# Kernel optimization log

Measured on AMD Instinct MI355X. Metric: run time of the kernel, lower is better.

Reference implementation:

```python
import jax, jax.numpy as jnp
import numpy as np

N, E, B = 100000, 1600000, 1024
F, H, C = 9, 4, 32
CH, L = 30, 20

def _leaky(x, slope):
    return jnp.where(x >= 0, x, slope * x)

def _add_self_loops(edge_index, n):
    ar = jnp.arange(n, dtype=edge_index.dtype)
    return jnp.concatenate([edge_index, jnp.stack([ar, ar])], axis=1)

def _gat_conv(x, edge_index, W, att_src, att_dst, bias):
    # PyG GATConv, concat heads, eval mode (no attn dropout), self loops
    n = x.shape[0]
    ei = _add_self_loops(edge_index, n)
    src, dst = ei[0], ei[1]
    h = (x @ W).reshape(n, H, C)                      # [N,H,C]
    a_s = jnp.sum(h * att_src, axis=-1)               # [N,H]
    a_d = jnp.sum(h * att_dst, axis=-1)               # [N,H]
    e = _leaky(a_s[src] + a_d[dst], 0.2)              # [Etot,H]
    m = jax.ops.segment_max(e, dst, num_segments=n)
    ex = jnp.exp(e - m[dst])
    s = jax.ops.segment_sum(ex, dst, num_segments=n)
    alpha = ex / (s[dst] + 1e-16)                     # softmax per dst node/head
    msg = h[src] * alpha[:, :, None]                  # [Etot,H,C]
    out = jax.ops.segment_sum(msg, dst, num_segments=n)
    return out.reshape(n, H * C) + bias

def _gcn_conv(x, edge_index, W, bias):
    # PyG GCNConv: self loops + symmetric normalization
    n = x.shape[0]
    ei = _add_self_loops(edge_index, n)
    src, dst = ei[0], ei[1]
    deg = jax.ops.segment_sum(jnp.ones(ei.shape[1], x.dtype), dst, num_segments=n)
    dinv = jnp.where(deg > 0, jax.lax.rsqrt(deg), 0.0)
    norm = dinv[src] * dinv[dst]                      # [Etot]
    h = x @ W
    out = jax.ops.segment_sum(h[src] * norm[:, None], dst, num_segments=n)
    return out + bias

def _global_mean_pool(x, batch, b):
    s = jax.ops.segment_sum(x, batch, num_segments=b)
    cnt = jax.ops.segment_sum(jnp.ones(x.shape[0], x.dtype), batch, num_segments=b)
    return s / jnp.maximum(cnt, 1.0)[:, None]

def _conv1d(x, w, b):
    # x: [B,Cin,L], w: [Cout,Cin,K], VALID conv
    y = jax.lax.conv_general_dilated(x, w, (1,), 'VALID',
                                     dimension_numbers=('NCH', 'OIH', 'NCH'))
    return y + b[None, :, None]

def _bn_eval(x, g, be, m, v):
    return (x - m[None, :, None]) * jax.lax.rsqrt(v[None, :, None] + 1e-5) * g[None, :, None] + be[None, :, None]

def _forward(x, seq_data, W_gat, att_src, att_dst, b_gat, W2, b2, W3, b3,
             conv1_w, conv1_b, conv2_w, conv2_b,
             bn1_g, bn1_b, bn1_m, bn1_v, bn2_g, bn2_b, bn2_m, bn2_v,
             fc1_W, fc1_b, fus_W, fus_b, cls1_W, cls1_b, cls3_W, cls3_b,
             edge_index, batch):
    slope = 0.01  # nn.LeakyReLU default
    # graph branch
    g = _leaky(_gat_conv(x, edge_index, W_gat, att_src, att_dst, b_gat), slope)
    g = _leaky(_gcn_conv(g, edge_index, W2, b2), slope)
    g = _leaky(_gcn_conv(g, edge_index, W3, b3), slope)
    g = _global_mean_pool(g, batch, B)                # [B,128]
    # sequence branch (eval mode: dropout = identity, BN uses running stats)
    s = _conv1d(seq_data, conv1_w, conv1_b)           # [B,64,18]
    s = _leaky(_bn_eval(s, bn1_g, bn1_b, bn1_m, bn1_v), slope)
    s = _conv1d(s, conv2_w, conv2_b)                  # [B,64,16]
    s = _leaky(_bn_eval(s, bn2_g, bn2_b, bn2_m, bn2_v), slope)
    s = s.reshape(s.shape[0], -1) @ fc1_W + fc1_b     # [B,64]
    # fusion + classifier
    comb = jnp.concatenate([g, s], axis=1)            # [B,192]
    comb = _leaky(comb @ fus_W + fus_b, slope)
    comb = _leaky(comb @ cls1_W + cls1_b, slope)
    return comb @ cls3_W + cls3_b                     # [B,1]

def setup_inputs():
    key = jax.random.key(0)
    ks = jax.random.split(key, 20)
    rn = lambda k, s, sc=0.1: jax.random.normal(k, s, dtype=jnp.float32) * sc
    return {
        'x': rn(ks[0], (N, F), 1.0),
        'edge_index': jax.random.randint(ks[1], (2, E), 0, N, dtype=jnp.int32),
        'batch': jnp.sort(jax.random.randint(ks[2], (N,), 0, B, dtype=jnp.int32)),
        'seq_data': rn(ks[3], (B, CH, L), 1.0),
        'W_gat': rn(ks[4], (F, H * C)), 'att_src': rn(ks[5], (H, C)),
        'att_dst': rn(ks[6], (H, C)), 'b_gat': jnp.zeros(H * C, jnp.float32),
        'W2': rn(ks[7], (H * C, 64)), 'b2': jnp.zeros(64, jnp.float32),
        'W3': rn(ks[8], (64, 128)), 'b3': jnp.zeros(128, jnp.float32),
        'conv1_w': rn(ks[9], (64, CH, 3)), 'conv1_b': jnp.zeros(64, jnp.float32),
        'conv2_w': rn(ks[10], (64, 64, 3)), 'conv2_b': jnp.zeros(64, jnp.float32),
        'bn1_g': jnp.ones(64, jnp.float32), 'bn1_b': jnp.zeros(64, jnp.float32),
        'bn1_m': jnp.zeros(64, jnp.float32), 'bn1_v': jnp.ones(64, jnp.float32),
        'bn2_g': jnp.ones(64, jnp.float32), 'bn2_b': jnp.zeros(64, jnp.float32),
        'bn2_m': jnp.zeros(64, jnp.float32), 'bn2_v': jnp.ones(64, jnp.float32),
        'fc1_W': rn(ks[11], (16 * 64, 64)), 'fc1_b': jnp.zeros(64, jnp.float32),
        'fus_W': rn(ks[12], (192, 128)), 'fus_b': jnp.zeros(128, jnp.float32),
        'cls1_W': rn(ks[13], (128, 64)), 'cls1_b': jnp.zeros(64, jnp.float32),
        'cls3_W': rn(ks[14], (64, 1)), 'cls3_b': jnp.zeros(1, jnp.float32),
    }

def reference(x, edge_index, batch, seq_data, W_gat, att_src, att_dst, b_gat,
              W2, b2, W3, b3, conv1_w, conv1_b, conv2_w, conv2_b,
              bn1_g, bn1_b, bn1_m, bn1_v, bn2_g, bn2_b, bn2_m, bn2_v,
              fc1_W, fc1_b, fus_W, fus_b, cls1_W, cls1_b, cls3_W, cls3_b):
    return _forward(x, seq_data, W_gat, att_src, att_dst, b_gat, W2, b2, W3, b3,
                    conv1_w, conv1_b, conv2_w, conv2_b,
                    bn1_g, bn1_b, bn1_m, bn1_v, bn2_g, bn2_b, bn2_m, bn2_v,
                    fc1_W, fc1_b, fus_W, fus_b, cls1_W, cls1_b, cls3_W, cls3_b,
                    edge_index, batch)
```

## Files before the change

### kernel.cpp

```cpp
#include <hip/hip_runtime.h>

#define NND 100000
#define NED 1600000
#define NB  1024
#define FEAT 9
#define HC 128
#define NBUCK ((NND + 511) / 512)
#define BCAP 12288u
#define BINCHUNK 4096
#define BIN_NBLK ((NED + BINCHUNK - 1) / BINCHUNK)

typedef unsigned short u16;

__device__ __forceinline__ void atomAdd(float* p, float v) {
    __hip_atomic_fetch_add(p, v, __ATOMIC_RELAXED, __HIP_MEMORY_SCOPE_AGENT);
}
__device__ __forceinline__ unsigned atomAddU(unsigned* p, unsigned v) {
    return __hip_atomic_fetch_add(p, v, __ATOMIC_RELAXED, __HIP_MEMORY_SCOPE_AGENT);
}
__device__ __forceinline__ float leaky(float v, float s) { return v >= 0.f ? v : s * v; }
__device__ __forceinline__ float bf2f(u16 u) {
    union { unsigned i; float f; } x; x.i = ((unsigned)u) << 16; return x.f;
}
__device__ __forceinline__ u16 f2bf(float f) {
    union { float f; unsigned i; } x; x.f = f;
    return (u16)((x.i + 0x7fffu + ((x.i >> 16) & 1u)) >> 16);
}
__device__ __forceinline__ float bflo(unsigned u) {
    union { unsigned i; float f; } x; x.i = u << 16; return x.f;
}
__device__ __forceinline__ float bfhi(unsigned u) {
    union { unsigned i; float f; } x; x.i = u & 0xffff0000u; return x.f;
}

__global__ void k_matt(const float* __restrict__ Wg, const float* __restrict__ attS,
                       const float* __restrict__ attD, float* __restrict__ M) {
    int t = threadIdx.x;
    if (t >= 72) return;
    int d = t >= 36 ? 1 : 0;
    int q = t - 36 * d;
    int f = q >> 2, h = q & 3;
    const float* av = d ? attD : attS;
    float s = 0.f;
#pragma unroll
    for (int c = 0; c < 32; ++c) s += Wg[f * HC + h * 32 + c] * av[h * 32 + c];
    M[d * 36 + q] = s;
}

__global__ void k_w2t(const float* __restrict__ W2, const float* __restrict__ W3,
                      u16* __restrict__ w2t, u16* __restrict__ w3t,
                      unsigned* __restrict__ bktCur) {
    int i = blockIdx.x * 256 + threadIdx.x;
    int n = i >> 7, k = i & 127;
    w2t[i] = f2bf(W2[k * 64 + n]);
    int n3 = i >> 6, k3 = i & 63;
    w3t[i] = f2bf(W3[k3 * 128 + n3]);
    if (i < NBUCK) bktCur[i] = (unsigned)i * BCAP;
}

__global__ void k_att(const float* __restrict__ x, const float* __restrict__ M,
                      u16* __restrict__ rec, float* __restrict__ a_d) {
    __shared__ float Ms[36], Md[36];
    int t = threadIdx.x;
    if (t < 36) Ms[t] = M[t];
    else if (t < 72) Md[t - 36] = M[t];
    __syncthreads();
    int n = blockIdx.x * 256 + t;
    if (n >= NND) return;
    float xv[FEAT];
#pragma unroll
    for (int f = 0; f < FEAT; ++f) xv[f] = x[n * FEAT + f];
    float s0 = 0, s1 = 0, s2 = 0, s3 = 0, d0 = 0, d1 = 0, d2 = 0, d3 = 0;
#pragma unroll
    for (int f = 0; f < FEAT; ++f) {
        float xf = xv[f];
        s0 += xf * Ms[f * 4 + 0]; s1 += xf * Ms[f * 4 + 1];
        s2 += xf * Ms[f * 4 + 2]; s3 += xf * Ms[f * 4 + 3];
        d0 += xf * Md[f * 4 + 0]; d1 += xf * Md[f * 4 + 1];
        d2 += xf * Md[f * 4 + 2]; d3 += xf * Md[f * 4 + 3];
    }
    u16 v[16];
#pragma unroll
    for (int f = 0; f < FEAT; ++f) v[f] = f2bf(xv[f]);
    v[9] = 0; v[10] = 0; v[11] = 0;
    v[12] = f2bf(s0); v[13] = f2bf(s1); v[14] = f2bf(s2); v[15] = f2bf(s3);
    unsigned pk[8];
#pragma unroll
    for (int i = 0; i < 8; ++i) pk[i] = (unsigned)v[2 * i] | ((unsigned)v[2 * i + 1] << 16);
    uint4* rp = (uint4*)(rec + (size_t)n * 16);
    rp[0] = make_uint4(pk[0], pk[1], pk[2], pk[3]);
    rp[1] = make_uint4(pk[4], pk[5], pk[6], pk[7]);
    ((float4*)a_d)[n] = make_float4(d0, d1, d2, d3);
}

__global__ __launch_bounds__(256) void k_bin(const int* __restrict__ ei,
                                             unsigned* __restrict__ bktCursor,
                                             unsigned* __restrict__ staging) {
    __shared__ unsigned hist[NBUCK];
    __shared__ unsigned gbase[NBUCK];
    int t = threadIdx.x;
    if (t < NBUCK) hist[t] = 0;
    __syncthreads();
    int base = blockIdx.x * BINCHUNK;
    int lim = NED - base;
    int srcv[16], dstv[16];
#pragma unroll
    for (int k = 0; k < 16; ++k) {
        int i = t + k * 256;
        if (i < lim) {
            srcv[k] = ei[base + i];
            dstv[k] = ei[NED + base + i];
            atomicAdd(&hist[dstv[k] >> 9], 1u);
        } else dstv[k] = -1;
    }
    __syncthreads();
    if (t < NBUCK) {
        unsigned c = hist[t];
        gbase[t] = c ? atomAddU(&bktCursor[t], c) : 0u;
    }
    __syncthreads();
    if (t < NBUCK) hist[t] = 0;
    __syncthreads();
#pragma unroll
    for (int k = 0; k < 16; ++k) {
        if (dstv[k] >= 0) {
            int bk = dstv[k] >> 9;
            unsigned off = atomicAdd(&hist[bk], 1u);
            staging[gbase[bk] + off] = ((unsigned)(dstv[k] & 511) << 17) | (unsigned)srcv[k];
        }
    }
}

__global__ __launch_bounds__(512) void k_place(const unsigned* __restrict__ bktCur,
                                               const unsigned* __restrict__ staging,
                                               unsigned* __restrict__ csr,
                                               unsigned* __restrict__ rowptr,
                                               u16* __restrict__ degA,
                                               float* __restrict__ dinv) {
    __shared__ unsigned lh[512];
    __shared__ unsigned ls[512];
    int b = blockIdx.x, t = threadIdx.x;
    unsigned lo = (unsigned)b * BCAP;
    unsigned n = bktCur[b] - lo;
    lh[t] = 0;
    __syncthreads();
    for (unsigned i = t; i < n; i += 512) atomicAdd(&lh[staging[lo + i] >> 17], 1u);
    __syncthreads();
    unsigned v = lh[t];
    ls[t] = v;
    __syncthreads();
    for (int off = 1; off < 512; off <<= 1) {
        unsigned u = (t >= off) ? ls[t - off] : 0u;
        __syncthreads();
        ls[t] += u;
        __syncthreads();
    }
    unsigned excl = ls[t] - v;
    int node = b * 512 + t;
    if (node < NND) {
        rowptr[node] = lo + excl;
        degA[node] = (u16)v;
        dinv[node] = rsqrtf((float)v + 1.f);
    }
    __syncthreads();
    lh[t] = excl;
    __syncthreads();
    for (unsigned i = t; i < n; i += 512) {
        unsigned p = staging[lo + i];
        unsigned pos = atomicAdd(&lh[p >> 17], 1u);
        csr[lo + pos] = p & 0x1FFFFu;
    }
}

__global__ __launch_bounds__(256) void k_gat_g(const unsigned* __restrict__ rowptr,
                                               const u16* __restrict__ degA,
                                               const unsigned* __restrict__ csr,
                                               const u16* __restrict__ rec,
                                               const float* __restrict__ a_d,
                                               float* __restrict__ z) {
    int n = blockIdx.x * 4 + (threadIdx.x >> 6);
    int l = threadIdx.x & 63;
    int e = l >> 2;
    int h = l & 3;
    unsigned e0 = rowptr[n];
    int m = (int)degA[n] + 1;
    float adh = a_d[n * 4 + h];
    float acc0 = 0, acc1 = 0, acc2 = 0, acc3 = 0, acc4 = 0, acc5 = 0, acc6 = 0, acc7 = 0, acc8 = 0;
    float den = 0.f;
    const uint4* recp = (const uint4*)rec;
    for (int c = 0; c < m; c += 16) {
        int idx = c + e;
        bool act = idx < m;
        int src = n;
        if (act && idx > 0) src = (int)csr[e0 + idx - 1];
        uint4 lo = recp[(size_t)src * 2];
        uint4 hi = recp[(size_t)src * 2 + 1];
        unsigned pair = (h & 2) ? hi.w : hi.z;
        float asf = (h & 1) ? bfhi(pair) : bflo(pair);
        float w = __expf(leaky(asf + adh, 0.2f));
        if (!act) w = 0.f;
        den += w;
        acc0 += w * bflo(lo.x); acc1 += w * bfhi(lo.x);
        acc2 += w * bflo(lo.y); acc3 += w * bfhi(lo.y);
        acc4 += w * bflo(lo.z); acc5 += w * bfhi(lo.z);
        acc6 += w * bflo(lo.w); acc7 += w * bfhi(lo.w);
        acc8 += w * bflo(hi.x);
    }
#pragma unroll
    for (int mask = 4; mask <= 32; mask <<= 1) {
        den  += __shfl_xor(den,  mask, 64);
        acc0 += __shfl_xor(acc0, mask, 64);
        acc1 += __shfl_xor(acc1, mask, 64);
        acc2 += __shfl_xor(acc2, mask, 64);
        acc3 += __shfl_xor(acc3, mask, 64);
        acc4 += __shfl_xor(acc4, mask, 64);
        acc5 += __shfl_xor(acc5, mask, 64);
        acc6 += __shfl_xor(acc6, mask, 64);
        acc7 += __shfl_xor(acc7, mask, 64);
        acc8 += __shfl_xor(acc8, mask, 64);
    }
    if (l < 4) {
        float inv = 1.f / (den + 1e-16f);
        float* zp = z + (size_t)n * 36 + h * 9;
        zp[0] = acc0 * inv; zp[1] = acc1 * inv; zp[2] = acc2 * inv;
        zp[3] = acc3 * inv; zp[4] = acc4 * inv; zp[5] = acc5 * inv;
        zp[6] = acc6 * inv; zp[7] = acc7 * inv; zp[8] = acc8 * inv;
    }
}

typedef __attribute__((ext_vector_type(8))) short bfrag;
typedef __attribute__((ext_vector_type(4))) float ffrag;
__global__ __launch_bounds__(256) void k_fused_h2(const float* __restrict__ z,
                                                  const float* __restrict__ Wg,
                                                  const float* __restrict__ bg,
                                                  const u16* __restrict__ w2t,
                                                  const float* __restrict__ dinv,
                                                  u16* __restrict__ h2) {
    __shared__ float zL[64 * 36];
    __shared__ float Wf[FEAT * HC];
    __shared__ float bgs[HC];
    __shared__ u16 g1L[64 * 136];
    int t = threadIdx.x;
    int n0 = blockIdx.x * 64;
    for (int i = t; i < 64 * 36; i += 256) {
        int row = i / 36;
        zL[i] = (n0 + row < NND) ? z[(size_t)(n0 + row) * 36 + (i - row * 36)] : 0.f;
    }
    for (int i = t; i < FEAT * HC; i += 256) Wf[i] = Wg[i];
    if (t < HC) bgs[t] = bg[t];
    __syncthreads();
    for (int e = t; e < 64 * 128; e += 256) {
        int row = e >> 7, col = e & 127;
        int h = col >> 5;
        float acc = bgs[col];
        const float* zr = zL + row * 36 + h * 9;
#pragma unroll
        for (int f = 0; f < 9; ++f) acc += zr[f] * Wf[f * 128 + col];
        g1L[row * 136 + col] = f2bf(leaky(acc, 0.01f));
    }
    __syncthreads();
    int l = t & 63, wv = t >> 6;
    int mr = l & 15, quad = l >> 4;
    union U { uint4 u; bfrag v; };
    bfrag a[4];
#pragma unroll
    for (int ks = 0; ks < 4; ++ks) {
        U uu; uu.u = *(const uint4*)(g1L + (wv * 16 + mr) * 136 + ks * 32 + quad * 8);
        a[ks] = uu.v;
    }
    ffrag acc[4];
#pragma unroll
    for (int ct = 0; ct < 4; ++ct) acc[ct] = (ffrag){0.f, 0.f, 0.f, 0.f};
#pragma unroll
    for (int ct = 0; ct < 4; ++ct) {
#pragma unroll
        for (int ks = 0; ks < 4; ++ks) {
            U ub; ub.u = *(const uint4*)(w2t + (ct * 16 + mr) * 128 + ks * 32 + quad * 8);
            acc[ct] = __builtin_amdgcn_mfma_f32_16x16x32_bf16(a[ks], ub.v, acc[ct], 0, 0, 0);
        }
    }
    int rbase = n0 + wv * 16 + quad * 4;
    if (rbase < NND) {
        float4 d4 = *(const float4*)(dinv + rbase);
        const float dv[4] = {d4.x, d4.y, d4.z, d4.w};
#pragma unroll
        for (int ct = 0; ct < 4; ++ct)
#pragma unroll
            for (int r = 0; r < 4; ++r)
                h2[(size_t)(rbase + r) * 64 + ct * 16 + mr] = f2bf(dv[r] * acc[ct][r]);
    }
}

template <int OUTMODE>
__global__ void k_gcn_g(const unsigned* __restrict__ rowptr, const u16* __restrict__ degA,
                        const unsigned* __restrict__ csr,
                        const float* __restrict__ dinv, const u16* __restrict__ hin,
                        const float* __restrict__ bias, u16* __restrict__ hout) {
    int n = blockIdx.x * 4 + (threadIdx.x >> 6);
    int l = threadIdx.x & 63;
    int grp = l >> 4;
    int c = l & 15;
    unsigned e0 = rowptr[n];
    unsigned e1 = e0 + degA[n];
    const uint2* hinU = (const uint2*)hin;
    float a0 = 0, a1 = 0, a2 = 0, a3 = 0;
    if (grp == 0) {
        uint2 u = hinU[(size_t)n * 16 + c];
        a0 = bflo(u.x); a1 = bfhi(u.x); a2 = bflo(u.y); a3 = bfhi(u.y);
    }
    unsigned e = e0;
    for (; e + 8 <= e1; e += 8) {
        unsigned s0 = csr[e + grp];
        unsigned s1 = csr[e + 4 + grp];
        uint2 u0 = hinU[(size_t)s0 * 16 + c];
        uint2 u1 = hinU[(size_t)s1 * 16 + c];
        a0 += bflo(u0.x) + bflo(u1.x); a1 += bfhi(u0.x) + bfhi(u1.x);
        a2 += bflo(u0.y) + bflo(u1.y); a3 += bfhi(u0.y) + bfhi(u1.y);
    }
    for (; e + 4 <= e1; e += 4) {
        unsigned s = csr[e + grp];
        uint2 u = hinU[(size_t)s * 16 + c];
        a0 += bflo(u.x); a1 += bfhi(u.x); a2 += bflo(u.y); a3 += bfhi(u.y);
    }
    if (grp < (int)(e1 - e)) {
        unsigned s = csr[e + grp];
        uint2 u = hinU[(size_t)s * 16 + c];
        a0 += bflo(u.x); a1 += bfhi(u.x); a2 += bflo(u.y); a3 += bfhi(u.y);
    }
#pragma unroll
    for (int mask = 16; mask <= 32; mask <<= 1) {
        a0 += __shfl_xor(a0, mask, 64);
        a1 += __shfl_xor(a1, mask, 64);
        a2 += __shfl_xor(a2, mask, 64);
        a3 += __shfl_xor(a3, mask, 64);
    }
    if (grp == 0) {
        float dn = dinv[n];
        float o0 = dn * a0, o1 = dn * a1, o2 = dn * a2, o3 = dn * a3;
        if (OUTMODE == 1) {
            o0 = leaky(o0 + bias[4 * c],     0.01f) * dn;
            o1 = leaky(o1 + bias[4 * c + 1], 0.01f) * dn;
            o2 = leaky(o2 + bias[4 * c + 2], 0.01f) * dn;
            o3 = leaky(o3 + bias[4 * c + 3], 0.01f) * dn;
        }
        uint2 pk;
        pk.x = (unsigned)f2bf(o0) | ((unsigned)f2bf(o1) << 16);
        pk.y = (unsigned)f2bf(o2) | ((unsigned)f2bf(o3) << 16);
        ((uint2*)hout)[(size_t)n * 16 + c] = pk;
    }
}

__global__ __launch_bounds__(256) void k_gcn2_pool(const u16* __restrict__ agg3,
                                                   const u16* __restrict__ w3t,
                                                   const float* __restrict__ b3,
                                                   const int* __restrict__ batch,
                                                   float* __restrict__ pooled,
                                                   float* __restrict__ cnt) {
    __shared__ u16 rows[64 * 72];
    __shared__ int bts[64];
    __shared__ float b3s[128];
    int t = threadIdx.x;
    int n0 = blockIdx.x * 64;
    int nn = NND - n0; if (nn > 64) nn = 64;
    const uint4* src = (const uint4*)(agg3 + (size_t)n0 * 64);
    for (int i = t; i < 512; i += 256) {
        int r = i >> 3, c8 = i & 7;
        uint4 v = (r < nn) ? src[i] : make_uint4(0u, 0u, 0u, 0u);
        *(uint4*)(rows + r * 72 + c8 * 8) = v;
    }
    if (t < 64) bts[t] = (t < nn) ? batch[n0 + t] : -1;
    if (t < 128) b3s[t] = b3[t];
    __syncthreads();
    int l = t & 63, wv = t >> 6;
    int mr = l & 15, quad = l >> 4;
    union U { uint4 u; bfrag v; };
    bfrag a[2];
#pragma unroll
    for (int ks = 0; ks < 2; ++ks) {
        U uu; uu.u = *(const uint4*)(rows + (wv * 16 + mr) * 72 + ks * 32 + quad * 8);
        a[ks] = uu.v;
    }
    ffrag acc[8];
#pragma unroll
    for (int ct = 0; ct < 8; ++ct) acc[ct] = (ffrag){0.f, 0.f, 0.f, 0.f};
#pragma unroll
    for (int ct = 0; ct < 8; ++ct) {
#pragma unroll
        for (int ks = 0; ks < 2; ++ks) {
            U ub; ub.u = *(const uint4*)(w3t + (ct * 16 + mr) * 64 + ks * 32 + quad * 8);
            acc[ct] = __builtin_amdgcn_mfma_f32_16x16x32_bf16(a[ks], ub.v, acc[ct], 0, 0, 0);
        }
    }
    int rl = wv * 16 + quad * 4;
    int ub = bts[wv * 16];
    bool uni = (ub == bts[wv * 16 + 15]);
#pragma unroll
    for (int ct = 0; ct < 8; ++ct) {
        int col = ct * 16 + mr;
        float bc = b3s[col];
        float g0 = leaky(acc[ct][0] + bc, 0.01f);
        float g1 = leaky(acc[ct][1] + bc, 0.01f);
        float g2 = leaky(acc[ct][2] + bc, 0.01f);
        float g3 = leaky(acc[ct][3] + bc, 0.01f);
        if (uni) {
            float s = g0 + g1 + g2 + g3;
            s += __shfl_xor(s, 16, 64);
            s += __shfl_xor(s, 32, 64);
            if (quad == 0 && ub >= 0) atomAdd(&pooled[ub * 128 + col], s);
        } else {
            float gr[4] = {g0, g1, g2, g3};
            int curb = bts[rl];
            float s = 0.f;
#pragma unroll
            for (int r = 0; r < 4; ++r) {
                int b = bts[rl + r];
                if (b != curb) {
                    if (curb >= 0) atomAdd(&pooled[curb * 128 + col], s);
                    s = 0.f; curb = b;
                }
                s += gr[r];
            }
            if (curb >= 0) atomAdd(&pooled[curb * 128 + col], s);
        }
    }
    if (t < nn) {
        int b = bts[t];
        if (t == 0 || bts[t - 1] != b) {
            int len = 1;
            for (int j = t + 1; j < nn && bts[j] == b; ++j) ++len;
            atomAdd(&cnt[b], (float)len);
        }
    }
}

__global__ void k_seq(const float* __restrict__ seq, const float* __restrict__ w1, const float* __restrict__ c1b,
                      const float* __restrict__ w2, const float* __restrict__ c2b,
                      const float* __restrict__ g1n, const float* __restrict__ b1n,
                      const float* __restrict__ m1n, const float* __restrict__ v1n,
                      const float* __restrict__ g2n, const float* __restrict__ b2n,
                      const float* __restrict__ m2n, const float* __restrict__ v2n,
                      const float* __restrict__ fcW, const float* __restrict__ fcb,
                      float* __restrict__ sfc) {
    __shared__ float xs[30 * 20];
    __shared__ float y1[64 * 18];
    __shared__ float y2[64 * 16];
    __shared__ float red[4][64];
    int t = threadIdx.x;
    int b = blockIdx.x;
    for (int idx = t; idx < 600; idx += 256) xs[idx] = seq[b * 600 + idx];
    __syncthreads();
    for (int idx = t; idx < 64 * 18; idx += 256) {
        int o = idx / 18, l = idx - o * 18;
        float acc = c1b[o];
        for (int i = 0; i < 30; ++i)
#pragma unroll
            for (int k = 0; k < 3; ++k)
                acc += xs[i * 20 + l + k] * w1[o * 90 + i * 3 + k];
        float bn = (acc - m1n[o]) * rsqrtf(v1n[o] + 1e-5f) * g1n[o] + b1n[o];
        y1[idx] = leaky(bn, 0.01f);
    }
    __syncthreads();
    for (int idx = t; idx < 64 * 16; idx += 256) {
        int o = idx >> 4, l = idx & 15;
        float acc = c2b[o];
        for (int i = 0; i < 64; ++i)
#pragma unroll
            for (int k = 0; k < 3; ++k)
                acc += y1[i * 18 + l + k] * w2[o * 192 + i * 3 + k];
        float bn = (acc - m2n[o]) * rsqrtf(v2n[o] + 1e-5f) * g2n[o] + b2n[o];
        y2[idx] = leaky(bn, 0.01f);
    }
    __syncthreads();
    {
        int o = t & 63, part = t >> 6;
        float acc = 0.f;
        for (int j = part * 256; j < part * 256 + 256; ++j)
            acc += y2[j] * fcW[j * 64 + o];
        red[part][o] = acc;
    }
    __syncthreads();
    if (t < 64) sfc[b * 64 + t] = red[0][t] + red[1][t] + red[2][t] + red[3][t] + fcb[t];
}

__global__ void k_final(const float* __restrict__ pooled, const float* __restrict__ cnt,
                        const float* __restrict__ sfc,
                        const float* __restrict__ fusW, const float* __restrict__ fusb,
                        const float* __restrict__ c1W, const float* __restrict__ c1b,
                        const float* __restrict__ c3W, const float* __restrict__ c3b,
                        float* __restrict__ out) {
    __shared__ float comb[192];
    __shared__ float t1[128];
    int t = threadIdx.x;
    int b = blockIdx.x;
    float invc = 1.f / fmaxf(cnt[b], 1.f);
    comb[t] = pooled[b * 128 + t] * invc;
    if (t < 64) comb[128 + t] = sfc[b * 64 + t];
    __syncthreads();
    float acc = fusb[t];
    for (int k = 0; k < 192; ++k) acc += comb[k] * fusW[k * 128 + t];
    t1[t] = leaky(acc, 0.01f);
    __syncthreads();
    if (t < 64) {
        float a2 = c1b[t];
        for (int k = 0; k < 128; ++k) a2 += t1[k] * c1W[k * 64 + t];
        a2 = leaky(a2, 0.01f);
        float p = a2 * c3W[t];
#pragma unroll
        for (int off = 32; off; off >>= 1) p += __shfl_xor(p, off, 64);
        if (t == 0) out[b] = p + c3b[0];
    }
}

extern "C" void kernel_launch(void* const* d_in, const int* in_sizes, int n_in,
                              void* d_out, int out_size, void* d_ws, size_t ws_size,
                              hipStream_t stream) {
    const float* x     = (const float*)d_in[0];
    const int*   ei    = (const int*)d_in[1];
    const int*   batch = (const int*)d_in[2];
    const float* seq   = (const float*)d_in[3];
    const float* Wg    = (const float*)d_in[4];
    const float* attS  = (const float*)d_in[5];
    const float* attD  = (const float*)d_in[6];
    const float* bg    = (const float*)d_in[7];
    const float* W2    = (const float*)d_in[8];
    const float* b2    = (const float*)d_in[9];
    const float* W3    = (const float*)d_in[10];
    const float* b3    = (const float*)d_in[11];
    const float* c1w   = (const float*)d_in[12];
    const float* c1bb  = (const float*)d_in[13];
    const float* c2w   = (const float*)d_in[14];
    const float* c2bb  = (const float*)d_in[15];
    const float* bn1g  = (const float*)d_in[16];
    const float* bn1b  = (const float*)d_in[17];
    const float* bn1m  = (const float*)d_in[18];
    const float* bn1v  = (const float*)d_in[19];
    const float* bn2g  = (const float*)d_in[20];
    const float* bn2b  = (const float*)d_in[21];
    const float* bn2m  = (const float*)d_in[22];
    const float* bn2v  = (const float*)d_in[23];
    const float* fcW   = (const float*)d_in[24];
    const float* fcb   = (const float*)d_in[25];
    const float* fusW  = (const float*)d_in[26];
    const float* fusb  = (const float*)d_in[27];
    const float* cls1W = (const float*)d_in[28];
    const float* cls1b = (const float*)d_in[29];
    const float* cls3W = (const float*)d_in[30];
    const float* cls3b = (const float*)d_in[31];

    char* wsb = (char*)d_ws;
    const size_t N = NND;
    float*    M      = (float*)wsb;
    float*    a_d    = M + 80;
    u16*      rec    = (u16*)(a_d + N * 4);
    float*    dinv   = (float*)(rec + N * 16);
    float*    pooled = dinv + N;
    float*    cnt    = pooled + (size_t)NB * 128;
    unsigned* bktCur = (unsigned*)(cnt + NB);
    unsigned* rowptr = bktCur + 256;
    u16*      degA   = (u16*)(rowptr + N);
    u16*      w2t    = degA + N + 8;
    u16*      w3t    = w2t + 8192;
    unsigned* staging= (unsigned*)(w3t + 8192);
    unsigned* csr    = staging + (size_t)NBUCK * BCAP;
    float*    z      = (float*)(csr + (size_t)NBUCK * BCAP);
    u16*      h2b    = (u16*)(z + N * 36 + 64);
    u16*      g2b    = h2b + N * 64;
    u16*      agg3b  = g2b + N * 64;
    float*    sfc    = (float*)(agg3b + N * 64);

    size_t zero_bytes = ((size_t)NB * 128 + NB) * 4;
    hipMemsetAsync(pooled, 0, zero_bytes, stream);

    k_matt<<<1, 128, 0, stream>>>(Wg, attS, attD, M);
    k_w2t<<<32, 256, 0, stream>>>(W2, W3, w2t, w3t, bktCur);
    k_att<<<(NND + 255) / 256, 256, 0, stream>>>(x, M, rec, a_d);
    k_bin<<<BIN_NBLK, 256, 0, stream>>>(ei, bktCur, staging);
    k_place<<<NBUCK, 512, 0, stream>>>(bktCur, staging, csr, rowptr, degA, dinv);
    k_gat_g<<<NND / 4, 256, 0, stream>>>(rowptr, degA, csr, rec, a_d, z);
    k_fused_h2<<<(NND + 63) / 64, 256, 0, stream>>>(z, Wg, bg, w2t, dinv, h2b);
    k_gcn_g<1><<<NND / 4, 256, 0, stream>>>(rowptr, degA, csr, dinv, h2b, b2, g2b);
    k_gcn_g<0><<<NND / 4, 256, 0, stream>>>(rowptr, degA, csr, dinv, g2b, b2, agg3b);
    k_gcn2_pool<<<(NND + 63) / 64, 256, 0, stream>>>(agg3b, w3t, b3, batch, pooled, cnt);
    k_seq<<<NB, 256, 0, stream>>>(seq, c1w, c1bb, c2w, c2bb, bn1g, bn1b, bn1m, bn1v,
                                  bn2g, bn2b, bn2m, bn2v, fcW, fcb, sfc);
    k_final<<<NB, 128, 0, stream>>>(pooled, cnt, sfc, fusW, fusb, cls1W, cls1b,
                                    cls3W, cls3b, (float*)d_out);
}
```

Measured before the change: 435.3 us.

## Fuse GAT gather into H2 GEMM and second GCN gather into pooling kernel

Merges the GAT attention gather with the following dense transform. Each 64-node block computes its aggregated features into shared memory as bf16 and then runs the Wg projection with MFMA, using a new padded bf16 Wg, instead of scalar FMAs. Likewise, the second GCN neighbor aggregation now runs inside the W3+pool kernel, which removes the z and agg3 intermediate buffers and two launches. The cost is less parallelism per block, since each wave processes 16 nodes serially. The GAT output is also rounded to bf16 before the projection, which adds precision loss.

```diff
diff --git a/kernel.cpp b/kernel.cpp
--- a/kernel.cpp
+++ b/kernel.cpp
@@ -33,6 +33,9 @@
     union { unsigned i; float f; } x; x.i = u & 0xffff0000u; return x.f;
 }
 
+typedef __attribute__((ext_vector_type(8))) short bfrag;
+typedef __attribute__((ext_vector_type(4))) float ffrag;
+
 __global__ void k_matt(const float* __restrict__ Wg, const float* __restrict__ attS,
                        const float* __restrict__ attD, float* __restrict__ M) {
     int t = threadIdx.x;
@@ -48,13 +51,17 @@
 }
 
 __global__ void k_w2t(const float* __restrict__ W2, const float* __restrict__ W3,
+                      const float* __restrict__ Wg,
                       u16* __restrict__ w2t, u16* __restrict__ w3t,
-                      unsigned* __restrict__ bktCur) {
+                      u16* __restrict__ wgt, unsigned* __restrict__ bktCur) {
     int i = blockIdx.x * 256 + threadIdx.x;
     int n = i >> 7, k = i & 127;
     w2t[i] = f2bf(W2[k * 64 + n]);
     int n3 = i >> 6, k3 = i & 63;
     w3t[i] = f2bf(W3[k3 * 128 + n3]);
+    int col = i >> 6, kk = i & 63;
+    int f = kk - 9 * (col >> 5);
+    wgt[i] = (f >= 0 && f < 9) ? f2bf(Wg[f * 128 + col]) : (u16)0;
     if (i < NBUCK) bktCur[i] = (unsigned)i * BCAP;
 }
 
@@ -172,126 +179,137 @@
     }
 }
 
-__global__ __launch_bounds__(256) void k_gat_g(const unsigned* __restrict__ rowptr,
-                                               const u16* __restrict__ degA,
-                                               const unsigned* __restrict__ csr,
-                                               const u16* __restrict__ rec,
-                                               const float* __restrict__ a_d,
-                                               float* __restrict__ z) {
-    int n = blockIdx.x * 4 + (threadIdx.x >> 6);
-    int l = threadIdx.x & 63;
-    int e = l >> 2;
-    int h = l & 3;
-    unsigned e0 = rowptr[n];
-    int m = (int)degA[n] + 1;
-    float adh = a_d[n * 4 + h];
-    float acc0 = 0, acc1 = 0, acc2 = 0, acc3 = 0, acc4 = 0, acc5 = 0, acc6 = 0, acc7 = 0, acc8 = 0;
-    float den = 0.f;
-    const uint4* recp = (const uint4*)rec;
-    for (int c = 0; c < m; c += 16) {
-        int idx = c + e;
-        bool act = idx < m;
-        int src = n;
-        if (act && idx > 0) src = (int)csr[e0 + idx - 1];
-        uint4 lo = recp[(size_t)src * 2];
-        uint4 hi = recp[(size_t)src * 2 + 1];
-        unsigned pair = (h & 2) ? hi.w : hi.z;
-        float asf = (h & 1) ? bfhi(pair) : bflo(pair);
-        float w = __expf(leaky(asf + adh, 0.2f));
-        if (!act) w = 0.f;
-        den += w;
-        acc0 += w * bflo(lo.x); acc1 += w * bfhi(lo.x);
-        acc2 += w * bflo(lo.y); acc3 += w * bfhi(lo.y);
-        acc4 += w * bflo(lo.z); acc5 += w * bfhi(lo.z);
-        acc6 += w * bflo(lo.w); acc7 += w * bfhi(lo.w);
-        acc8 += w * bflo(hi.x);
-    }
-#pragma unroll
-    for (int mask = 4; mask <= 32; mask <<= 1) {
-        den  += __shfl_xor(den,  mask, 64);
-        acc0 += __shfl_xor(acc0, mask, 64);
-        acc1 += __shfl_xor(acc1, mask, 64);
-        acc2 += __shfl_xor(acc2, mask, 64);
-        acc3 += __shfl_xor(acc3, mask, 64);
-        acc4 += __shfl_xor(acc4, mask, 64);
-        acc5 += __shfl_xor(acc5, mask, 64);
-        acc6 += __shfl_xor(acc6, mask, 64);
-        acc7 += __shfl_xor(acc7, mask, 64);
-        acc8 += __shfl_xor(acc8, mask, 64);
-    }
-    if (l < 4) {
-        float inv = 1.f / (den + 1e-16f);
-        float* zp = z + (size_t)n * 36 + h * 9;
-        zp[0] = acc0 * inv; zp[1] = acc1 * inv; zp[2] = acc2 * inv;
-        zp[3] = acc3 * inv; zp[4] = acc4 * inv; zp[5] = acc5 * inv;
-        zp[6] = acc6 * inv; zp[7] = acc7 * inv; zp[8] = acc8 * inv;
-    }
-}
-
-typedef __attribute__((ext_vector_type(8))) short bfrag;
-typedef __attribute__((ext_vector_type(4))) float ffrag;
-__global__ __launch_bounds__(256) void k_fused_h2(const float* __restrict__ z,
-                                                  const float* __restrict__ Wg,
-                                                  const float* __restrict__ bg,
-                                                  const u16* __restrict__ w2t,
-                                                  const float* __restrict__ dinv,
-                                                  u16* __restrict__ h2) {
-    __shared__ float zL[64 * 36];
-    __shared__ float Wf[FEAT * HC];
+__global__ __launch_bounds__(256) void k_gat_h2(const unsigned* __restrict__ rowptr,
+                                                const u16* __restrict__ degA,
+                                                const unsigned* __restrict__ csr,
+                                                const u16* __restrict__ rec,
+                                                const float* __restrict__ a_d,
+                                                const u16* __restrict__ wgt,
+                                                const float* __restrict__ bgv,
+                                                const u16* __restrict__ w2t,
+                                                const float* __restrict__ dinv,
+                                                u16* __restrict__ h2) {
+    __shared__ u16 zA[64 * 72];
+    __shared__ u16 g1L[64 * 136];
     __shared__ float bgs[HC];
-    __shared__ u16 g1L[64 * 136];
     int t = threadIdx.x;
     int n0 = blockIdx.x * 64;
-    for (int i = t; i < 64 * 36; i += 256) {
-        int row = i / 36;
-        zL[i] = (n0 + row < NND) ? z[(size_t)(n0 + row) * 36 + (i - row * 36)] : 0.f;
-    }
-    for (int i = t; i < FEAT * HC; i += 256) Wf[i] = Wg[i];
-    if (t < HC) bgs[t] = bg[t];
-    __syncthreads();
-    for (int e = t; e < 64 * 128; e += 256) {
-        int row = e >> 7, col = e & 127;
-        int h = col >> 5;
-        float acc = bgs[col];
-        const float* zr = zL + row * 36 + h * 9;
-#pragma unroll
-        for (int f = 0; f < 9; ++f) acc += zr[f] * Wf[f * 128 + col];
-        g1L[row * 136 + col] = f2bf(leaky(acc, 0.01f));
-    }
+    for (int i = t; i < 64 * 36; i += 256) ((unsigned*)zA)[i] = 0u;
+    if (t < HC) bgs[t] = bgv[t];
     __syncthreads();
     int l = t & 63, wv = t >> 6;
+    {
+        int e = l >> 2, h = l & 3;
+        const uint4* recp = (const uint4*)rec;
+        for (int j = 0; j < 16; ++j) {
+            int n = n0 + wv * 16 + j;
+            if (n >= NND) break;
+            unsigned e0 = rowptr[n];
+            int m = (int)degA[n] + 1;
+            float adh = a_d[n * 4 + h];
+            float acc0 = 0, acc1 = 0, acc2 = 0, acc3 = 0, acc4 = 0,
+                  acc5 = 0, acc6 = 0, acc7 = 0, acc8 = 0, den = 0.f;
+            for (int c = 0; c < m; c += 16) {
+                int idx = c + e;
+                bool act = idx < m;
+                int src = n;
+                if (act && idx > 0) src = (int)csr[e0 + idx - 1];
+                uint4 lo = recp[(size_t)src * 2];
+                uint4 hi = recp[(size_t)src * 2 + 1];
+                unsigned pair = (h & 2) ? hi.w : hi.z;
+                float asf = (h & 1) ? bfhi(pair) : bflo(pair);
+                float w = __expf(leaky(asf + adh, 0.2f));
+                if (!act) w = 0.f;
+                den += w;
+                acc0 += w * bflo(lo.x); acc1 += w * bfhi(lo.x);
+                acc2 += w * bflo(lo.y); acc3 += w * bfhi(lo.y);
+                acc4 += w * bflo(lo.z); acc5 += w * bfhi(lo.z);
+                acc6 += w * bflo(lo.w); acc7 += w * bfhi(lo.w);
+                acc8 += w * bflo(hi.x);
+            }
+#pragma unroll
+            for (int mask = 4; mask <= 32; mask <<= 1) {
+                den  += __shfl_xor(den,  mask, 64);
+                acc0 += __shfl_xor(acc0, mask, 64);
+                acc1 += __shfl_xor(acc1, mask, 64);
+                acc2 += __shfl_xor(acc2, mask, 64);
+                acc3 += __shfl_xor(acc3, mask, 64);
+                acc4 += __shfl_xor(acc4, mask, 64);
+                acc5 += __shfl_xor(acc5, mask, 64);
+                acc6 += __shfl_xor(acc6, mask, 64);
+                acc7 += __shfl_xor(acc7, mask, 64);
+                acc8 += __shfl_xor(acc8, mask, 64);
+            }
+            if (l < 4) {
+                float inv = 1.f / (den + 1e-16f);
+                u16* zp = zA + (wv * 16 + j) * 72 + l * 9;
+                zp[0] = f2bf(acc0 * inv); zp[1] = f2bf(acc1 * inv);
+                zp[2] = f2bf(acc2 * inv); zp[3] = f2bf(acc3 * inv);
+                zp[4] = f2bf(acc4 * inv); zp[5] = f2bf(acc5 * inv);
+                zp[6] = f2bf(acc6 * inv); zp[7] = f2bf(acc7 * inv);
+                zp[8] = f2bf(acc8 * inv);
+            }
+        }
+    }
+    __syncthreads();
     int mr = l & 15, quad = l >> 4;
     union U { uint4 u; bfrag v; };
-    bfrag a[4];
-#pragma unroll
-    for (int ks = 0; ks < 4; ++ks) {
-        U uu; uu.u = *(const uint4*)(g1L + (wv * 16 + mr) * 136 + ks * 32 + quad * 8);
-        a[ks] = uu.v;
-    }
-    ffrag acc[4];
-#pragma unroll
-    for (int ct = 0; ct < 4; ++ct) acc[ct] = (ffrag){0.f, 0.f, 0.f, 0.f};
-#pragma unroll
-    for (int ct = 0; ct < 4; ++ct) {
+    {
+        bfrag a[2];
+#pragma unroll
+        for (int ks = 0; ks < 2; ++ks) {
+            U uu; uu.u = *(const uint4*)(zA + (wv * 16 + mr) * 72 + ks * 32 + quad * 8);
+            a[ks] = uu.v;
+        }
+#pragma unroll
+        for (int ct = 0; ct < 8; ++ct) {
+            ffrag c = (ffrag){0.f, 0.f, 0.f, 0.f};
+#pragma unroll
+            for (int ks = 0; ks < 2; ++ks) {
+                U ub; ub.u = *(const uint4*)(wgt + (ct * 16 + mr) * 64 + ks * 32 + quad * 8);
+                c = __builtin_amdgcn_mfma_f32_16x16x32_bf16(a[ks], ub.v, c, 0, 0, 0);
+            }
+            int col = ct * 16 + mr;
+            float bc = bgs[col];
+#pragma unroll
+            for (int r = 0; r < 4; ++r) {
+                int row = wv * 16 + quad * 4 + r;
+                g1L[row * 136 + col] = f2bf(leaky(c[r] + bc, 0.01f));
+            }
+        }
+    }
+    __syncthreads();
+    {
+        bfrag a[4];
 #pragma unroll
         for (int ks = 0; ks < 4; ++ks) {
-            U ub; ub.u = *(const uint4*)(w2t + (ct * 16 + mr) * 128 + ks * 32 + quad * 8);
-            acc[ct] = __builtin_amdgcn_mfma_f32_16x16x32_bf16(a[ks], ub.v, acc[ct], 0, 0, 0);
-        }
-    }
-    int rbase = n0 + wv * 16 + quad * 4;
-    if (rbase < NND) {
-        float4 d4 = *(const float4*)(dinv + rbase);
-        const float dv[4] = {d4.x, d4.y, d4.z, d4.w};
-#pragma unroll
-        for (int ct = 0; ct < 4; ++ct)
-#pragma unroll
-            for (int r = 0; r < 4; ++r)
-                h2[(size_t)(rbase + r) * 64 + ct * 16 + mr] = f2bf(dv[r] * acc[ct][r]);
-    }
-}
-
-template <int OUTMODE>
+            U uu; uu.u = *(const uint4*)(g1L + (wv * 16 + mr) * 136 + ks * 32 + quad * 8);
+            a[ks] = uu.v;
+        }
+        ffrag acc[4];
+#pragma unroll
+        for (int ct = 0; ct < 4; ++ct) acc[ct] = (ffrag){0.f, 0.f, 0.f, 0.f};
+#pragma unroll
+        for (int ct = 0; ct < 4; ++ct) {
+#pragma unroll
+            for (int ks = 0; ks < 4; ++ks) {
+                U ub; ub.u = *(const uint4*)(w2t + (ct * 16 + mr) * 128 + ks * 32 + quad * 8);
+                acc[ct] = __builtin_amdgcn_mfma_f32_16x16x32_bf16(a[ks], ub.v, acc[ct], 0, 0, 0);
+            }
+        }
+        int rbase = n0 + wv * 16 + quad * 4;
+        if (rbase < NND) {
+            float4 d4 = *(const float4*)(dinv + rbase);
+            const float dv[4] = {d4.x, d4.y, d4.z, d4.w};
+#pragma unroll
+            for (int ct = 0; ct < 4; ++ct)
+#pragma unroll
+                for (int r = 0; r < 4; ++r)
+                    h2[(size_t)(rbase + r) * 64 + ct * 16 + mr] = f2bf(dv[r] * acc[ct][r]);
+        }
+    }
+}
+
 __global__ void k_gcn_g(const unsigned* __restrict__ rowptr, const u16* __restrict__ degA,
                         const unsigned* __restrict__ csr,
                         const float* __restrict__ dinv, const u16* __restrict__ hin,
@@ -336,13 +354,10 @@
     }
     if (grp == 0) {
         float dn = dinv[n];
-        float o0 = dn * a0, o1 = dn * a1, o2 = dn * a2, o3 = dn * a3;
-        if (OUTMODE == 1) {
-            o0 = leaky(o0 + bias[4 * c],     0.01f) * dn;
-            o1 = leaky(o1 + bias[4 * c + 1], 0.01f) * dn;
-            o2 = leaky(o2 + bias[4 * c + 2], 0.01f) * dn;
-            o3 = leaky(o3 + bias[4 * c + 3], 0.01f) * dn;
-        }
+        float o0 = leaky(dn * a0 + bias[4 * c],     0.01f) * dn;
+        float o1 = leaky(dn * a1 + bias[4 * c + 1], 0.01f) * dn;
+        float o2 = leaky(dn * a2 + bias[4 * c + 2], 0.01f) * dn;
+        float o3 = leaky(dn * a3 + bias[4 * c + 3], 0.01f) * dn;
         uint2 pk;
         pk.x = (unsigned)f2bf(o0) | ((unsigned)f2bf(o1) << 16);
         pk.y = (unsigned)f2bf(o2) | ((unsigned)f2bf(o3) << 16);
@@ -350,28 +365,76 @@
     }
 }
 
-__global__ __launch_bounds__(256) void k_gcn2_pool(const u16* __restrict__ agg3,
-                                                   const u16* __restrict__ w3t,
-                                                   const float* __restrict__ b3,
-                                                   const int* __restrict__ batch,
-                                                   float* __restrict__ pooled,
-                                                   float* __restrict__ cnt) {
+__global__ __launch_bounds__(256) void k_gcn2_fused(const unsigned* __restrict__ rowptr,
+                                                    const u16* __restrict__ degA,
+                                                    const unsigned* __restrict__ csr,
+                                                    const float* __restrict__ dinv,
+                                                    const u16* __restrict__ g2b,
+                                                    const u16* __restrict__ w3t,
+                                                    const float* __restrict__ b3,
+                                                    const int* __restrict__ batch,
+                                                    float* __restrict__ pooled,
+                                                    float* __restrict__ cnt) {
     __shared__ u16 rows[64 * 72];
     __shared__ int bts[64];
     __shared__ float b3s[128];
     int t = threadIdx.x;
     int n0 = blockIdx.x * 64;
     int nn = NND - n0; if (nn > 64) nn = 64;
-    const uint4* src = (const uint4*)(agg3 + (size_t)n0 * 64);
-    for (int i = t; i < 512; i += 256) {
-        int r = i >> 3, c8 = i & 7;
-        uint4 v = (r < nn) ? src[i] : make_uint4(0u, 0u, 0u, 0u);
-        *(uint4*)(rows + r * 72 + c8 * 8) = v;
-    }
+    for (int i = t; i < 64 * 36; i += 256) ((unsigned*)rows)[i] = 0u;
     if (t < 64) bts[t] = (t < nn) ? batch[n0 + t] : -1;
     if (t < 128) b3s[t] = b3[t];
     __syncthreads();
     int l = t & 63, wv = t >> 6;
+    {
+        int grp = l >> 4, c = l & 15;
+        const uint2* hinU = (const uint2*)g2b;
+        for (int j = 0; j < 16; ++j) {
+            int n = n0 + wv * 16 + j;
+            if (n >= NND) break;
+            unsigned e0 = rowptr[n];
+            unsigned e1 = e0 + degA[n];
+            float a0 = 0, a1 = 0, a2 = 0, a3 = 0;
+            if (grp == 0) {
+                uint2 u = hinU[(size_t)n * 16 + c];
+                a0 = bflo(u.x); a1 = bfhi(u.x); a2 = bflo(u.y); a3 = bfhi(u.y);
+            }
+            unsigned e = e0;
+            for (; e + 8 <= e1; e += 8) {
+                unsigned s0 = csr[e + grp];
+                unsigned s1 = csr[e + 4 + grp];
+                uint2 u0 = hinU[(size_t)s0 * 16 + c];
+                uint2 u1 = hinU[(size_t)s1 * 16 + c];
+                a0 += bflo(u0.x) + bflo(u1.x); a1 += bfhi(u0.x) + bfhi(u1.x);
+                a2 += bflo(u0.y) + bflo(u1.y); a3 += bfhi(u0.y) + bfhi(u1.y);
+            }
+            for (; e + 4 <= e1; e += 4) {
+                unsigned s = csr[e + grp];
+                uint2 u = hinU[(size_t)s * 16 + c];
+                a0 += bflo(u.x); a1 += bfhi(u.x); a2 += bflo(u.y); a3 += bfhi(u.y);
+            }
+            if (grp < (int)(e1 - e)) {
+                unsigned s = csr[e + grp];
+                uint2 u = hinU[(size_t)s * 16 + c];
+                a0 += bflo(u.x); a1 += bfhi(u.x); a2 += bflo(u.y); a3 += bfhi(u.y);
+            }
+#pragma unroll
+            for (int mask = 16; mask <= 32; mask <<= 1) {
+                a0 += __shfl_xor(a0, mask, 64);
+                a1 += __shfl_xor(a1, mask, 64);
+                a2 += __shfl_xor(a2, mask, 64);
+                a3 += __shfl_xor(a3, mask, 64);
+            }
+            if (grp == 0) {
+                float dn = dinv[n];
+                uint2 pk;
+                pk.x = (unsigned)f2bf(dn * a0) | ((unsigned)f2bf(dn * a1) << 16);
+                pk.y = (unsigned)f2bf(dn * a2) | ((unsigned)f2bf(dn * a3) << 16);
+                *(uint2*)(rows + (wv * 16 + j) * 72 + c * 4) = pk;
+            }
+        }
+    }
+    __syncthreads();
     int mr = l & 15, quad = l >> 4;
     union U { uint4 u; bfrag v; };
     bfrag a[2];
@@ -560,27 +623,26 @@
     u16*      degA   = (u16*)(rowptr + N);
     u16*      w2t    = degA + N + 8;
     u16*      w3t    = w2t + 8192;
-    unsigned* staging= (unsigned*)(w3t + 8192);
+    u16*      wgt    = w3t + 8192;
+    unsigned* staging= (unsigned*)(wgt + 8192);
     unsigned* csr    = staging + (size_t)NBUCK * BCAP;
-    float*    z      = (float*)(csr + (size_t)NBUCK * BCAP);
-    u16*      h2b    = (u16*)(z + N * 36 + 64);
+    u16*      h2b    = (u16*)(csr + (size_t)NBUCK * BCAP);
     u16*      g2b    = h2b + N * 64;
-    u16*      agg3b  = g2b + N * 64;
-    float*    sfc    = (float*)(agg3b + N * 64);
+    float*    sfc    = (float*)(g2b + N * 64);
 
     size_t zero_bytes = ((size_t)NB * 128 + NB) * 4;
     hipMemsetAsync(pooled, 0, zero_bytes, stream);
 
     k_matt<<<1, 128, 0, stream>>>(Wg, attS, attD, M);
-    k_w2t<<<32, 256, 0, stream>>>(W2, W3, w2t, w3t, bktCur);
+    k_w2t<<<32, 256, 0, stream>>>(W2, W3, Wg, w2t, w3t, wgt, bktCur);
     k_att<<<(NND + 255) / 256, 256, 0, stream>>>(x, M, rec, a_d);
     k_bin<<<BIN_NBLK, 256, 0, stream>>>(ei, bktCur, staging);
     k_place<<<NBUCK, 512, 0, stream>>>(bktCur, staging, csr, rowptr, degA, dinv);
-    k_gat_g<<<NND / 4, 256, 0, stream>>>(rowptr, degA, csr, rec, a_d, z);
-    k_fused_h2<<<(NND + 63) / 64, 256, 0, stream>>>(z, Wg, bg, w2t, dinv, h2b);
-    k_gcn_g<1><<<NND / 4, 256, 0, stream>>>(rowptr, degA, csr, dinv, h2b, b2, g2b);
-    k_gcn_g<0><<<NND / 4, 256, 0, stream>>>(rowptr, degA, csr, dinv, g2b, b2, agg3b);
-    k_gcn2_pool<<<(NND + 63) / 64, 256, 0, stream>>>(agg3b, w3t, b3, batch, pooled, cnt);
+    k_gat_h2<<<(NND + 63) / 64, 256, 0, stream>>>(rowptr, degA, csr, rec, a_d,
+                                                  wgt, bg, w2t, dinv, h2b);
+    k_gcn_g<<<NND / 4, 256, 0, stream>>>(rowptr, degA, csr, dinv, h2b, b2, g2b);
+    k_gcn2_fused<<<(NND + 63) / 64, 256, 0, stream>>>(rowptr, degA, csr, dinv, g2b,
+                                                      w3t, b3, batch, pooled, cnt);
     k_seq<<<NB, 256, 0, stream>>>(seq, c1w, c1bb, c2w, c2bb, bn1g, bn1b, bn1m, bn1v,
                                   bn2g, bn2b, bn2m, bn2v, fcW, fcb, sfc);
     k_final<<<NB, 128, 0, stream>>>(pooled, cnt, sfc, fusW, fusb, cls1W, cls1b,
```

New measurement: 476.9 us. 9.6% more time.

## Store GAT aggregate as bf16 and compute GAT projection with MFMA

Applied to the files above, without the earlier changes.

The GAT aggregation output z is now written as bf16 instead of fp32, which halves its write and read traffic. The per-head 9x32 projection in k_fused_h2 was a scalar FMA loop. It becomes an MFMA matmul against a block-diagonal bf16 weight matrix (64x128, zero-padded per head) that k_w2t prepares. The cost is extra bf16 rounding of z and of the GAT weights, and wasted MFMA work on the zero blocks.

```diff
diff --git a/kernel.cpp b/kernel.cpp
--- a/kernel.cpp
+++ b/kernel.cpp
@@ -33,6 +33,9 @@
     union { unsigned i; float f; } x; x.i = u & 0xffff0000u; return x.f;
 }
 
+typedef __attribute__((ext_vector_type(8))) short bfrag;
+typedef __attribute__((ext_vector_type(4))) float ffrag;
+
 __global__ void k_matt(const float* __restrict__ Wg, const float* __restrict__ attS,
                        const float* __restrict__ attD, float* __restrict__ M) {
     int t = threadIdx.x;
@@ -48,13 +51,17 @@
 }
 
 __global__ void k_w2t(const float* __restrict__ W2, const float* __restrict__ W3,
+                      const float* __restrict__ Wg,
                       u16* __restrict__ w2t, u16* __restrict__ w3t,
-                      unsigned* __restrict__ bktCur) {
+                      u16* __restrict__ wgt, unsigned* __restrict__ bktCur) {
     int i = blockIdx.x * 256 + threadIdx.x;
     int n = i >> 7, k = i & 127;
     w2t[i] = f2bf(W2[k * 64 + n]);
     int n3 = i >> 6, k3 = i & 63;
     w3t[i] = f2bf(W3[k3 * 128 + n3]);
+    int col = i >> 6, kk = i & 63;
+    int f = kk - 9 * (col >> 5);
+    wgt[i] = (f >= 0 && f < 9) ? f2bf(Wg[f * 128 + col]) : (u16)0;
     if (i < NBUCK) bktCur[i] = (unsigned)i * BCAP;
 }
 
@@ -177,7 +184,7 @@
                                                const unsigned* __restrict__ csr,
                                                const u16* __restrict__ rec,
                                                const float* __restrict__ a_d,
-                                               float* __restrict__ z) {
+                                               u16* __restrict__ zb) {
     int n = blockIdx.x * 4 + (threadIdx.x >> 6);
     int l = threadIdx.x & 63;
     int e = l >> 2;
@@ -221,73 +228,90 @@
     }
     if (l < 4) {
         float inv = 1.f / (den + 1e-16f);
-        float* zp = z + (size_t)n * 36 + h * 9;
-        zp[0] = acc0 * inv; zp[1] = acc1 * inv; zp[2] = acc2 * inv;
-        zp[3] = acc3 * inv; zp[4] = acc4 * inv; zp[5] = acc5 * inv;
-        zp[6] = acc6 * inv; zp[7] = acc7 * inv; zp[8] = acc8 * inv;
-    }
-}
-
-typedef __attribute__((ext_vector_type(8))) short bfrag;
-typedef __attribute__((ext_vector_type(4))) float ffrag;
-__global__ __launch_bounds__(256) void k_fused_h2(const float* __restrict__ z,
-                                                  const float* __restrict__ Wg,
-                                                  const float* __restrict__ bg,
+        u16* zp = zb + (size_t)n * 36 + h * 9;
+        zp[0] = f2bf(acc0 * inv); zp[1] = f2bf(acc1 * inv); zp[2] = f2bf(acc2 * inv);
+        zp[3] = f2bf(acc3 * inv); zp[4] = f2bf(acc4 * inv); zp[5] = f2bf(acc5 * inv);
+        zp[6] = f2bf(acc6 * inv); zp[7] = f2bf(acc7 * inv); zp[8] = f2bf(acc8 * inv);
+    }
+}
+
+__global__ __launch_bounds__(256) void k_fused_h2(const u16* __restrict__ zb,
+                                                  const u16* __restrict__ wgt,
+                                                  const float* __restrict__ bgv,
                                                   const u16* __restrict__ w2t,
                                                   const float* __restrict__ dinv,
                                                   u16* __restrict__ h2) {
-    __shared__ float zL[64 * 36];
-    __shared__ float Wf[FEAT * HC];
+    __shared__ u16 zA[64 * 72];
+    __shared__ u16 g1L[64 * 136];
     __shared__ float bgs[HC];
-    __shared__ u16 g1L[64 * 136];
     int t = threadIdx.x;
     int n0 = blockIdx.x * 64;
-    for (int i = t; i < 64 * 36; i += 256) {
-        int row = i / 36;
-        zL[i] = (n0 + row < NND) ? z[(size_t)(n0 + row) * 36 + (i - row * 36)] : 0.f;
-    }
-    for (int i = t; i < FEAT * HC; i += 256) Wf[i] = Wg[i];
-    if (t < HC) bgs[t] = bg[t];
-    __syncthreads();
-    for (int e = t; e < 64 * 128; e += 256) {
-        int row = e >> 7, col = e & 127;
-        int h = col >> 5;
-        float acc = bgs[col];
-        const float* zr = zL + row * 36 + h * 9;
-#pragma unroll
-        for (int f = 0; f < 9; ++f) acc += zr[f] * Wf[f * 128 + col];
-        g1L[row * 136 + col] = f2bf(leaky(acc, 0.01f));
+    int nn = NND - n0; if (nn > 64) nn = 64;
+    for (int i = t; i < 64 * 36; i += 256) ((unsigned*)zA)[i] = 0u;
+    if (t < HC) bgs[t] = bgv[t];
+    __syncthreads();
+    const unsigned* zbG = (const unsigned*)zb;
+    for (int i = t; i < nn * 18; i += 256) {
+        int r = i / 18, c = i - r * 18;
+        ((unsigned*)zA)[r * 36 + c] = zbG[(size_t)(n0 + r) * 18 + c];
     }
     __syncthreads();
     int l = t & 63, wv = t >> 6;
     int mr = l & 15, quad = l >> 4;
     union U { uint4 u; bfrag v; };
-    bfrag a[4];
-#pragma unroll
-    for (int ks = 0; ks < 4; ++ks) {
-        U uu; uu.u = *(const uint4*)(g1L + (wv * 16 + mr) * 136 + ks * 32 + quad * 8);
-        a[ks] = uu.v;
-    }
-    ffrag acc[4];
-#pragma unroll
-    for (int ct = 0; ct < 4; ++ct) acc[ct] = (ffrag){0.f, 0.f, 0.f, 0.f};
-#pragma unroll
-    for (int ct = 0; ct < 4; ++ct) {
+    {
+        bfrag a[2];
+#pragma unroll
+        for (int ks = 0; ks < 2; ++ks) {
+            U uu; uu.u = *(const uint4*)(zA + (wv * 16 + mr) * 72 + ks * 32 + quad * 8);
+            a[ks] = uu.v;
+        }
+#pragma unroll
+        for (int ct = 0; ct < 8; ++ct) {
+            ffrag c = (ffrag){0.f, 0.f, 0.f, 0.f};
+#pragma unroll
+            for (int ks = 0; ks < 2; ++ks) {
+                U ub; ub.u = *(const uint4*)(wgt + (ct * 16 + mr) * 64 + ks * 32 + quad * 8);
+                c = __builtin_amdgcn_mfma_f32_16x16x32_bf16(a[ks], ub.v, c, 0, 0, 0);
+            }
+            int col = ct * 16 + mr;
+            float bc = bgs[col];
+#pragma unroll
+            for (int r = 0; r < 4; ++r) {
+                int row = wv * 16 + quad * 4 + r;
+                g1L[row * 136 + col] = f2bf(leaky(c[r] + bc, 0.01f));
+            }
+        }
+    }
+    __syncthreads();
+    {
+        bfrag a[4];
 #pragma unroll
         for (int ks = 0; ks < 4; ++ks) {
-            U ub; ub.u = *(const uint4*)(w2t + (ct * 16 + mr) * 128 + ks * 32 + quad * 8);
-            acc[ct] = __builtin_amdgcn_mfma_f32_16x16x32_bf16(a[ks], ub.v, acc[ct], 0, 0, 0);
-        }
-    }
-    int rbase = n0 + wv * 16 + quad * 4;
-    if (rbase < NND) {
-        float4 d4 = *(const float4*)(dinv + rbase);
-        const float dv[4] = {d4.x, d4.y, d4.z, d4.w};
-#pragma unroll
-        for (int ct = 0; ct < 4; ++ct)
-#pragma unroll
-            for (int r = 0; r < 4; ++r)
-                h2[(size_t)(rbase + r) * 64 + ct * 16 + mr] = f2bf(dv[r] * acc[ct][r]);
+            U uu; uu.u = *(const uint4*)(g1L + (wv * 16 + mr) * 136 + ks * 32 + quad * 8);
+            a[ks] = uu.v;
+        }
+        ffrag acc[4];
+#pragma unroll
+        for (int ct = 0; ct < 4; ++ct) acc[ct] = (ffrag){0.f, 0.f, 0.f, 0.f};
+#pragma unroll
+        for (int ct = 0; ct < 4; ++ct) {
+#pragma unroll
+            for (int ks = 0; ks < 4; ++ks) {
+                U ub; ub.u = *(const uint4*)(w2t + (ct * 16 + mr) * 128 + ks * 32 + quad * 8);
+                acc[ct] = __builtin_amdgcn_mfma_f32_16x16x32_bf16(a[ks], ub.v, acc[ct], 0, 0, 0);
+            }
+        }
+        int rbase = n0 + wv * 16 + quad * 4;
+        if (rbase < NND) {
+            float4 d4 = *(const float4*)(dinv + rbase);
+            const float dv[4] = {d4.x, d4.y, d4.z, d4.w};
+#pragma unroll
+            for (int ct = 0; ct < 4; ++ct)
+#pragma unroll
+                for (int r = 0; r < 4; ++r)
+                    h2[(size_t)(rbase + r) * 64 + ct * 16 + mr] = f2bf(dv[r] * acc[ct][r]);
+        }
     }
 }
 
@@ -560,10 +584,11 @@
     u16*      degA   = (u16*)(rowptr + N);
     u16*      w2t    = degA + N + 8;
     u16*      w3t    = w2t + 8192;
-    unsigned* staging= (unsigned*)(w3t + 8192);
+    u16*      wgt    = w3t + 8192;
+    unsigned* staging= (unsigned*)(wgt + 8192);
     unsigned* csr    = staging + (size_t)NBUCK * BCAP;
-    float*    z      = (float*)(csr + (size_t)NBUCK * BCAP);
-    u16*      h2b    = (u16*)(z + N * 36 + 64);
+    u16*      zb     = (u16*)(csr + (size_t)NBUCK * BCAP);
+    u16*      h2b    = zb + N * 36 + 16;
     u16*      g2b    = h2b + N * 64;
     u16*      agg3b  = g2b + N * 64;
     float*    sfc    = (float*)(agg3b + N * 64);
@@ -572,12 +597,12 @@
     hipMemsetAsync(pooled, 0, zero_bytes, stream);
 
     k_matt<<<1, 128, 0, stream>>>(Wg, attS, attD, M);
-    k_w2t<<<32, 256, 0, stream>>>(W2, W3, w2t, w3t, bktCur);
+    k_w2t<<<32, 256, 0, stream>>>(W2, W3, Wg, w2t, w3t, wgt, bktCur);
     k_att<<<(NND + 255) / 256, 256, 0, stream>>>(x, M, rec, a_d);
     k_bin<<<BIN_NBLK, 256, 0, stream>>>(ei, bktCur, staging);
     k_place<<<NBUCK, 512, 0, stream>>>(bktCur, staging, csr, rowptr, degA, dinv);
-    k_gat_g<<<NND / 4, 256, 0, stream>>>(rowptr, degA, csr, rec, a_d, z);
-    k_fused_h2<<<(NND + 63) / 64, 256, 0, stream>>>(z, Wg, bg, w2t, dinv, h2b);
+    k_gat_g<<<NND / 4, 256, 0, stream>>>(rowptr, degA, csr, rec, a_d, zb);
+    k_fused_h2<<<(NND + 63) / 64, 256, 0, stream>>>(zb, wgt, bg, w2t, dinv, h2b);
     k_gcn_g<1><<<NND / 4, 256, 0, stream>>>(rowptr, degA, csr, dinv, h2b, b2, g2b);
     k_gcn_g<0><<<NND / 4, 256, 0, stream>>>(rowptr, degA, csr, dinv, g2b, b2, agg3b);
     k_gcn2_pool<<<(NND + 63) / 64, 256, 0, stream>>>(agg3b, w3t, b3, batch, pooled, cnt);
```

New measurement: 441.0 us. About the same (+1.3%).
